# Kernel tuning notes

Hardware: AMD Instinct MI355X
Metric: run time of the kernel (lower is better)

The kernel has to match this reference:

```python
import jax, jax.numpy as jnp
import numpy as np

U = 256    # hp.hidden_size * 2 (attention num_units / encoder dim)
H = 128    # hp.hidden_size (prenet output, attn GRU input)
MEL = 80   # hp.decoder_output_dim == hp.num_mels
R = 5      # hp.outputs_per_step
B = 64
T = 1000


def _glorot(key, shape):
    fan_in = shape[-1]
    return jax.random.normal(key, shape, jnp.float32) / jnp.sqrt(jnp.float32(fan_in))


def setup_inputs() -> dict:
    key = jax.random.key(0)
    ks = jax.random.split(key, 16)
    p = {}
    p["memory"] = jax.random.normal(ks[0], (B, T, U), jnp.float32)
    # prenet: fc1 (MEL->U), fc2 (U->H)
    p["Wp1"] = _glorot(ks[1], (U, MEL)); p["bp1"] = jnp.zeros((U,), jnp.float32)
    p["Wp2"] = _glorot(ks[2], (H, U));   p["bp2"] = jnp.zeros((H,), jnp.float32)
    # Bahdanau attention params (no bias)
    p["W1"] = _glorot(ks[3], (U, U))
    p["W2"] = _glorot(ks[4], (U, U))
    p["v"]  = _glorot(ks[5], (U,))
    def gru(k, din):
        k1, k2 = jax.random.split(k)
        return (_glorot(k1, (3 * U, din)), _glorot(k2, (3 * U, U)),
                jnp.zeros((3 * U,), jnp.float32), jnp.zeros((3 * U,), jnp.float32))
    p["Wa_ih"], p["Wa_hh"], p["ba_ih"], p["ba_hh"] = gru(ks[6], H)
    p["W1_ih"], p["W1_hh"], p["b1_ih"], p["b1_hh"] = gru(ks[7], U)
    p["W2_ih"], p["W2_hh"], p["b2_ih"], p["b2_hh"] = gru(ks[8], U)
    p["Wproj"] = _glorot(ks[9], (U, 2 * U)); p["bproj"] = jnp.zeros((U,), jnp.float32)
    p["Wout"] = _glorot(ks[10], (MEL * R, U)); p["bout"] = jnp.zeros((MEL * R,), jnp.float32)
    return p


def _gru_cell(x, h, W_ih, W_hh, b_ih, b_hh):
    # torch.nn.GRUCell semantics
    gi = x @ W_ih.T + b_ih
    gh = h @ W_hh.T + b_hh
    ir, iz, inn = jnp.split(gi, 3, axis=-1)
    hr, hz, hn = jnp.split(gh, 3, axis=-1)
    r = jax.nn.sigmoid(ir + hr)
    z = jax.nn.sigmoid(iz + hz)
    n = jnp.tanh(inn + r * hn)
    return (1.0 - z) * n + z * h


def reference(memory, Wp1, bp1, Wp2, bp2, W1, W2, v,
              Wa_ih, Wa_hh, ba_ih, ba_hh,
              W1_ih, W1_hh, b1_ih, b1_hh,
              W2_ih, W2_hh, b2_ih, b2_hh,
              Wproj, bproj, Wout, bout):
    b, t, u = memory.shape
    steps = t // R  # training branch: timesteps = memory_len // outputs_per_step
    # keys = W1(memory): constant across timesteps, hoist out of the loop
    keys = jnp.einsum('btu,vu->btv', memory, W1)
    init = (jnp.zeros((b, MEL), memory.dtype),  # prev mel frame (GO frame = zeros)
            jnp.zeros((b, u), memory.dtype),    # attn_hidden
            jnp.zeros((b, u), memory.dtype),    # gru1_hidden
            jnp.zeros((b, u), memory.dtype))    # gru2_hidden

    def step(carry, _):
        prev, attn_h, g1_h, g2_h = carry
        # prenet (dropout omitted for determinism; identity in eval mode)
        x = jax.nn.relu(prev @ Wp1.T + bp1)
        x = jax.nn.relu(x @ Wp2.T + bp2)
        # attention query through GRU cell
        d_t = _gru_cell(x, attn_h, Wa_ih, Wa_hh, ba_ih, ba_hh)
        q = d_t @ W2.T                                     # [b,u]
        scores = jnp.tanh(keys + q[:, None, :]) @ v       # [b,t]
        aw = jax.nn.softmax(scores, axis=1)
        d_t_prime = jnp.einsum('bt,btu->bu', aw, memory)   # context
        # residual GRU stack
        g1_in = jnp.concatenate([d_t, d_t_prime], axis=1) @ Wproj.T + bproj
        g1_h = _gru_cell(g1_in, g1_h, W1_ih, W1_hh, b1_ih, b1_hh)
        g2_in = g1_in + g1_h
        g2_h = _gru_cell(g2_in, g2_h, W2_ih, W2_hh, b2_ih, b2_hh)
        out = ((g2_in + g2_h) @ Wout.T + bout).reshape(b, MEL, R)
        return (out[:, :, -1], d_t, g1_h, g2_h), out

    _, ys = jax.lax.scan(step, init, None, length=steps)   # [steps,b,MEL,R]
    # torch.cat(outputs, 2) -> [b, MEL, steps*R]
    return jnp.transpose(ys, (1, 2, 0, 3)).reshape(b, MEL, steps * R)
```

## Files before the change

### kernel.cpp

```cpp
#include <hip/hip_runtime.h>

typedef _Float16 f16;
typedef _Float16 h2 __attribute__((ext_vector_type(2)));
typedef float fv4 __attribute__((ext_vector_type(4)));

#define BB 64
#define UU 256
#define RRR 5
#define NQUAD 4

constexpr size_t O_WP1T = 0;
constexpr size_t O_WP2T = 10240;
constexpr size_t O_WAIH = 26624;
constexpr size_t O_WAHH = 75776;
constexpr size_t O_WQP  = 174080;
constexpr size_t O_WPC  = 239616;
constexpr size_t O_W1IH = 272384;
constexpr size_t O_W1HH = 370688;
constexpr size_t O_W2IH = 468992;
constexpr size_t O_W2HH = 567296;
constexpr size_t O_WOUT = 665600;
constexpr size_t OF_BQP = 716800;
constexpr size_t OF_W1T = 717312;
constexpr size_t OH_KEYS = 1565696;
constexpr size_t OH_MEM  = OH_KEYS + 16384000;
constexpr size_t OF_CTXP  = 17166848;
constexpr size_t OF_ESUM  = 17297920;
constexpr size_t OI_FLAGS = 17298432;

#define SCL2LOG2E 2.8853900817779268f

#if defined(__has_builtin)
#if __has_builtin(__builtin_amdgcn_fdot2)
#define USE_FDOT2 1
#endif
#endif

__device__ __forceinline__ float dot2f(h2 a, h2 b, float c){
#ifdef USE_FDOT2
  return __builtin_amdgcn_fdot2(a, b, c, false);
#else
  return c + (float)a[0]*(float)b[0] + (float)a[1]*(float)b[1];
#endif
}

__device__ __forceinline__ float frcp(float x){ return __builtin_amdgcn_rcpf(x); }
__device__ __forceinline__ float fexp2(float x){ return __builtin_amdgcn_exp2f(x); }
__device__ __forceinline__ float fsig(float x){ return frcp(1.0f + fexp2(-1.4426950408889634f*x)); }
__device__ __forceinline__ float ftanh(float x){ return 1.0f - 2.0f*frcp(1.0f + fexp2(SCL2LOG2E*x)); }

__global__ void k_tr_hx(const float* __restrict__ src, int srcK, int kbase,
                        h2* __restrict__ dst, int N, int K, int Ntot, int coloff,
                        float scale){
  int idx = blockIdx.x*blockDim.x + threadIdx.x;
  int tot = N*(K/2);
  if (idx < tot){
    int k2 = idx / N, n = idx - k2*N;
    h2 p; p[0]=(f16)(scale*src[n*srcK + kbase + 2*k2]);
    p[1]=(f16)(scale*src[n*srcK + kbase + 2*k2+1]);
    dst[(size_t)k2*Ntot + coloff + n] = p;
  }
}

__global__ void k_transpose(const float* __restrict__ src, float* __restrict__ dst, int N, int K){
  int idx = blockIdx.x*blockDim.x + threadIdx.x;
  if (idx < N*K){
    int n = idx / K, k = idx - n*K;
    dst[k*N + n] = src[idx];
  }
}

__global__ void k_biasqp(const float* __restrict__ bproj, float* __restrict__ dst){
  int i = blockIdx.x*blockDim.x + threadIdx.x;
  if (i < 512) dst[i] = (i < 256) ? 0.f : bproj[i-256];
}

__global__ void k_zero(int* __restrict__ p, int n){
  int i = blockIdx.x*blockDim.x + threadIdx.x;
  if (i < n) p[i] = 0;
}

__global__ void k_memh(const float* __restrict__ src, f16* __restrict__ dst, int n8){
  int i = blockIdx.x*blockDim.x + threadIdx.x;
  if (i < n8){
    const float4* s = reinterpret_cast<const float4*>(src) + 2*(size_t)i;
    float4 f0 = s[0], f1 = s[1];
    union { f16 h[8]; float4 v; } u;
    u.h[0]=(f16)f0.x; u.h[1]=(f16)f0.y; u.h[2]=(f16)f0.z; u.h[3]=(f16)f0.w;
    u.h[4]=(f16)f1.x; u.h[5]=(f16)f1.y; u.h[6]=(f16)f1.z; u.h[7]=(f16)f1.w;
    reinterpret_cast<float4*>(dst)[i] = u.v;
  }
}

__global__ __launch_bounds__(256) void k_keys(const float* __restrict__ mem,
      const float* __restrict__ W1t, f16* __restrict__ keys, int T)
{
  const int b = blockIdx.z;
  const int tbase = blockIdx.x * 128;
  const int cbase = blockIdx.y * 128;
  const int tid = threadIdx.x;
  const int rt = tid >> 4, ct = tid & 15;
  const float* memb = mem + (size_t)b*T*UU;

  float acc[8][8];
  #pragma unroll
  for (int i=0;i<8;i++){
    #pragma unroll
    for (int j=0;j<8;j++) acc[i][j]=0.f;
  }
  const float* arow[8];
  #pragma unroll
  for (int i=0;i<8;i++){
    int t = tbase + rt*8 + i;
    arow[i] = memb + (size_t)(t < T ? t : T-1)*UU;
  }
  const float* wcol = W1t + cbase + ct*8;

  for (int k=0;k<UU;k+=4){
    float w8[4][8];
    #pragma unroll
    for (int kk=0;kk<4;kk++){
      float4 lo = *reinterpret_cast<const float4*>(wcol + (size_t)(k+kk)*UU);
      float4 hi = *reinterpret_cast<const float4*>(wcol + (size_t)(k+kk)*UU + 4);
      w8[kk][0]=lo.x; w8[kk][1]=lo.y; w8[kk][2]=lo.z; w8[kk][3]=lo.w;
      w8[kk][4]=hi.x; w8[kk][5]=hi.y; w8[kk][6]=hi.z; w8[kk][7]=hi.w;
    }
    #pragma unroll
    for (int i=0;i<8;i++){
      float4 a = *reinterpret_cast<const float4*>(arow[i] + k);
      float a4[4] = {a.x, a.y, a.z, a.w};
      #pragma unroll
      for (int kk=0;kk<4;kk++){
        #pragma unroll
        for (int j=0;j<8;j++) acc[i][j] += a4[kk]*w8[kk][j];
      }
    }
  }
  #pragma unroll
  for (int i=0;i<8;i++){
    int t = tbase + rt*8 + i;
    if (t < T){
      f16* dst = keys + (size_t)b*T*UU + (size_t)t*UU + cbase + ct*8;
      union { f16 h[8]; float4 v; } u;
      #pragma unroll
      for (int j=0;j<8;j++) u.h[j] = (f16)(acc[i][j]*SCL2LOG2E);
      *reinterpret_cast<float4*>(dst) = u.v;
    }
  }
}

__device__ __attribute__((noinline)) void gemv_stage(
    const h2* __restrict__ W, const h2* __restrict__ in,
    const float* __restrict__ bias, float* __restrict__ dest, h2* __restrict__ desth,
    float* __restrict__ spart, int K2, int Nf4, int j4shift, int act, int tid)
{
  const int j4cap = 1 << j4shift;
  const int ksn   = 1024 >> j4shift;
  const int j4 = tid & (j4cap - 1);
  const int ks = tid >> j4shift;
  float4* part4 = reinterpret_cast<float4*>(spart);
  if (j4 < Nf4){
    int k2a = (K2 * ks) / ksn;
    int k2b = (K2 * (ks+1)) / ksn;
    const float4* w = reinterpret_cast<const float4*>(W) + (size_t)k2a * Nf4 + j4;
    float a0=0.f, a1=0.f, a2=0.f, a3=0.f;
    #pragma unroll 4
    for (int k2 = k2a; k2 < k2b; ++k2){
      float4 wp = *w; w += Nf4;
      h2 a = in[k2];
      const h2* wh = reinterpret_cast<const h2*>(&wp);
      a0 = dot2f(wh[0], a, a0);
      a1 = dot2f(wh[1], a, a1);
      a2 = dot2f(wh[2], a, a2);
      a3 = dot2f(wh[3], a, a3);
    }
    float4 r; r.x=a0; r.y=a1; r.z=a2; r.w=a3;
    part4[ks * j4cap + j4] = r;
  }
  __syncthreads();
  if (tid < Nf4){
    float4 s = part4[tid];
    for (int k = 1; k < ksn; ++k){
      float4 p = part4[k * j4cap + tid];
      s.x+=p.x; s.y+=p.y; s.z+=p.z; s.w+=p.w;
    }
    if (bias){
      float4 bv = reinterpret_cast<const float4*>(bias)[tid];
      s.x+=bv.x; s.y+=bv.y; s.z+=bv.z; s.w+=bv.w;
    }
    if (act == 1){
      s.x=fmaxf(s.x,0.f); s.y=fmaxf(s.y,0.f); s.z=fmaxf(s.z,0.f); s.w=fmaxf(s.w,0.f);
    } else if (act == 2){
      float4 d = reinterpret_cast<float4*>(dest)[tid];
      s.x+=d.x; s.y+=d.y; s.z+=d.z; s.w+=d.w;
    }
    if (dest) reinterpret_cast<float4*>(dest)[tid] = s;
    if (desth){
      h2 p0; p0[0]=(f16)s.x; p0[1]=(f16)s.y;
      h2 p1; p1[0]=(f16)s.z; p1[1]=(f16)s.w;
      desth[2*tid] = p0; desth[2*tid+1] = p1;
    }
  }
  __syncthreads();
}

__device__ __attribute__((noinline)) void gru_gate(
    const float* __restrict__ gi, const float* __restrict__ gh,
    float* __restrict__ h, h2* __restrict__ hh2,
    const float* __restrict__ addsrc, float* __restrict__ sumf,
    h2* __restrict__ sumh, int tid)
{
  if (tid < 128){
    float hn[2], sm[2] = {0.f, 0.f};
    #pragma unroll
    for (int d=0; d<2; ++d){
      int e = 2*tid + d;
      float r = fsig(gi[e] + gh[e]);
      float z = fsig(gi[256+e] + gh[256+e]);
      float n = ftanh(gi[512+e] + r*gh[512+e]);
      hn[d] = (1.f - z)*n + z*h[e];
      h[e] = hn[d];
      if (addsrc){ sm[d] = addsrc[e] + hn[d]; if (sumf) sumf[e] = sm[d]; }
    }
    h2 p; p[0]=(f16)hn[0]; p[1]=(f16)hn[1];
    hh2[tid] = p;
    if (addsrc && sumh){ h2 q; q[0]=(f16)sm[0]; q[1]=(f16)sm[1]; sumh[tid] = q; }
  }
  __syncthreads();
}

__global__ __launch_bounds__(1024) void k_decode(
    const h2* __restrict__ wts, const float* __restrict__ wsf,
    const f16* __restrict__ keysg, const f16* __restrict__ memg,
    float* __restrict__ ctxp, float* __restrict__ esum, int* __restrict__ flags,
    const float* __restrict__ bp1, const float* __restrict__ bp2,
    const float* __restrict__ vvec,
    const float* __restrict__ ba_ih, const float* __restrict__ ba_hh,
    const float* __restrict__ b1_ih, const float* __restrict__ b1_hh,
    const float* __restrict__ b2_ih, const float* __restrict__ b2_hh,
    const float* __restrict__ bout,
    float* __restrict__ out, int T, int steps)
{
  __shared__ __align__(16) float s_part[4096];
  __shared__ __align__(16) float s_sc[1024];
  __shared__ __align__(16) float s_gi[768];
  __shared__ __align__(16) float s_gh[768];
  __shared__ __align__(16) float s_gh1[768];
  __shared__ __align__(16) float s_gh2[768];
  __shared__ __align__(16) float s_q[512];
  __shared__ __align__(16) float s_ha[256];
  __shared__ __align__(16) float s_g1h[256];
  __shared__ __align__(16) float s_g2h[256];
  __shared__ __align__(16) float s_g2in[256];
  __shared__ __align__(16) float s_y[400];
  __shared__ __align__(16) f16   s_prevf[80];
  __shared__ __align__(16) h2    s_hah[128], s_g1hh[128], s_g2hh[128];
  __shared__ __align__(16) h2    s_g1inh[128], s_g2inh[128], s_s2h[128];
  __shared__ __align__(16) h2    s_x1h[128], s_xh[64], s_ctxh[128];
  __shared__ float s_wred[16];

  const int b    = blockIdx.x & 63;
  const int quad = blockIdx.x >> 6;
  const int tid = threadIdx.x;
  const int lane = tid & 63;
  const int wid = tid >> 6;
  const int half_id = lane >> 5;
  const int cl = lane & 31;

  const f16* keyb = keysg + (size_t)b*T*UU;
  const f16* memb = memg  + (size_t)b*T*UU;
  float* outb = out + (size_t)b*80*(steps*RRR);
  const int tq0 = (T*quad)/NQUAD, tq1 = (T*(quad+1))/NQUAD;

  if (tid < 128){
    s_ha[2*tid]=0.f; s_ha[2*tid+1]=0.f;
    s_g1h[2*tid]=0.f; s_g1h[2*tid+1]=0.f;
    s_g2h[2*tid]=0.f; s_g2h[2*tid+1]=0.f;
    h2 z; z[0]=(f16)0.f; z[1]=(f16)0.f;
    s_hah[tid]=z; s_g1hh[tid]=z; s_g2hh[tid]=z;
  }
  if (tid < 80) s_prevf[tid] = (f16)0.f;
  __syncthreads();

  float v8[8], m8[8];
  #pragma unroll
  for (int j=0;j<8;j++){ v8[j] = vvec[cl*8+j]; m8[j] = -2.0f*v8[j]; }
  float sumv = 0.f;
  #pragma unroll
  for (int j=0;j<8;j++) sumv += v8[j];
  #pragma unroll
  for (int o=1;o<32;o<<=1) sumv += __shfl_xor(sumv, o);

  for (int step = 0; step < steps; ++step){
    const int par = step & 1;
    gemv_stage(wts+O_WAHH, s_hah,  ba_hh, s_gh,  nullptr, s_part, 128, 192, 8, 0, tid);
    gemv_stage(wts+O_W1HH, s_g1hh, b1_hh, s_gh1, nullptr, s_part, 128, 192, 8, 0, tid);
    gemv_stage(wts+O_W2HH, s_g2hh, b2_hh, s_gh2, nullptr, s_part, 128, 192, 8, 0, tid);
    gemv_stage(wts+O_WP1T, reinterpret_cast<const h2*>(s_prevf), bp1, nullptr, s_x1h,
               s_part, 40, 64, 6, 1, tid);
    gemv_stage(wts+O_WP2T, s_x1h, bp2, nullptr, s_xh, s_part, 128, 32, 5, 1, tid);
    gemv_stage(wts+O_WAIH, s_xh, ba_ih, s_gi, nullptr, s_part, 64, 192, 8, 0, tid);
    gru_gate(s_gi, s_gh, s_ha, s_hah, nullptr, nullptr, nullptr, tid);
    gemv_stage(wts+O_WQP, s_hah, wsf+OF_BQP, s_q, nullptr, s_part, 128, 128, 7, 0, tid);

    {
      float q8[8];
      #pragma unroll
      for (int j=0;j<8;j++) q8[j] = s_q[cl*8+j];
      float rs = 0.f;
      for (int t0 = tq0 + wid*2; t0 < tq1; t0 += 32){
        int t = t0 + half_id;
        fv4 kv = *(reinterpret_cast<const fv4*>(keyb + (size_t)t*UU) + cl);
        const h2* kh = reinterpret_cast<const h2*>(&kv);
        float acc = 0.f;
        #pragma unroll
        for (int p=0;p<4;p++){
          float t0f = (float)kh[p][0] + q8[2*p];
          float t1f = (float)kh[p][1] + q8[2*p+1];
          acc = fmaf(m8[2*p],   frcp(1.f + fexp2(t0f)), acc);
          acc = fmaf(m8[2*p+1], frcp(1.f + fexp2(t1f)), acc);
        }
        #pragma unroll
        for (int o=1;o<32;o<<=1) acc += __shfl_xor(acc, o);
        float e = __expf(sumv + acc);
        if (cl == 0) s_sc[t] = e;
        rs += e;
      }
      rs += __shfl_xor(rs, 32);
      if (lane==0) s_wred[wid] = rs;
    }
    __syncthreads();
    {
      float c8[8] = {0.f,0.f,0.f,0.f,0.f,0.f,0.f,0.f};
      for (int t0 = tq0 + wid*2; t0 < tq1; t0 += 32){
        int t = t0 + half_id;
        float wgt = s_sc[t];
        fv4 mv = *(reinterpret_cast<const fv4*>(memb + (size_t)t*UU) + cl);
        const h2* mh = reinterpret_cast<const h2*>(&mv);
        #pragma unroll
        for (int p=0;p<4;p++){
          c8[2*p  ] += wgt*(float)mh[p][0];
          c8[2*p+1] += wgt*(float)mh[p][1];
        }
      }
      #pragma unroll
      for (int j=0;j<8;j++) c8[j] += __shfl_xor(c8[j], 32);
      if (half_id == 0){
        float4 lo; lo.x=c8[0]; lo.y=c8[1]; lo.z=c8[2]; lo.w=c8[3];
        float4 hi; hi.x=c8[4]; hi.y=c8[5]; hi.z=c8[6]; hi.w=c8[7];
        *reinterpret_cast<float4*>(s_part + wid*256 + cl*8)     = lo;
        *reinterpret_cast<float4*>(s_part + wid*256 + cl*8 + 4) = hi;
      }
    }
    __syncthreads();
    {
      float* cp = ctxp + (((size_t)b*2 + par)*NQUAD + quad)*256;
      if (tid < 128){
        float a = 0.f, c = 0.f;
        #pragma unroll
        for (int w=0; w<16; ++w){
          a += s_part[w*256 + 2*tid];
          c += s_part[w*256 + 2*tid+1];
        }
        cp[2*tid]   = a;
        cp[2*tid+1] = c;
      }
      if (tid == 0){
        float tot = 0.f;
        #pragma unroll
        for (int w=0; w<16; ++w) tot += s_wred[w];
        esum[((size_t)b*2 + par)*NQUAD + quad] = tot;
      }
    }
    __syncthreads();
    if (tid == 0){
      int* fl = flags + b*256 + step;
      __threadfence();
      __hip_atomic_fetch_add(fl, 1, __ATOMIC_RELEASE, __HIP_MEMORY_SCOPE_AGENT);
      while (__hip_atomic_load(fl, __ATOMIC_ACQUIRE, __HIP_MEMORY_SCOPE_AGENT) < NQUAD){
        __builtin_amdgcn_s_sleep(2);
      }
    }
    __syncthreads();
    if (tid < 128){
      const float* cp0 = ctxp + ((size_t)b*2 + par)*NQUAD*256;
      const float* es0 = esum + ((size_t)b*2 + par)*NQUAD;
      float es = 0.f;
      #pragma unroll
      for (int q4=0;q4<NQUAD;q4++)
        es += __hip_atomic_load(&es0[q4], __ATOMIC_RELAXED, __HIP_MEMORY_SCOPE_AGENT);
      float inv = frcp(es);
      float a = 0.f, c = 0.f;
      #pragma unroll
      for (int q4=0;q4<NQUAD;q4++){
        a += __hip_atomic_load(&cp0[q4*256 + 2*tid],   __ATOMIC_RELAXED, __HIP_MEMORY_SCOPE_AGENT);
        c += __hip_atomic_load(&cp0[q4*256 + 2*tid+1], __ATOMIC_RELAXED, __HIP_MEMORY_SCOPE_AGENT);
      }
      h2 p; p[0]=(f16)(a*inv); p[1]=(f16)(c*inv);
      s_ctxh[tid] = p;
    }
    __syncthreads();

    gemv_stage(wts+O_WPC, s_ctxh, nullptr, s_q+256, s_g1inh, s_part, 128, 64, 6, 2, tid);
    gemv_stage(wts+O_W1IH, s_g1inh, b1_ih, s_gi, nullptr, s_part, 128, 192, 8, 0, tid);
    gru_gate(s_gi, s_gh1, s_g1h, s_g1hh, s_q+256, s_g2in, s_g2inh, tid);
    gemv_stage(wts+O_W2IH, s_g2inh, b2_ih, s_gi, nullptr, s_part, 128, 192, 8, 0, tid);
    gru_gate(s_gi, s_gh2, s_g2h, s_g2hh, s_g2in, nullptr, s_s2h, tid);
    gemv_stage(wts+O_WOUT, s_s2h, bout, s_y, nullptr, s_part, 128, 100, 7, 0, tid);
    if (tid < 400){
      float val = s_y[tid];
      int mel = tid / 5, rr = tid - mel*5;
      if (quad == 0)
        __builtin_nontemporal_store(val, &outb[(size_t)mel*(steps*RRR) + step*RRR + rr]);
      if (rr == 4) s_prevf[mel] = (f16)val;
    }
    __syncthreads();
  }
}

extern "C" void kernel_launch(void* const* d_in, const int* in_sizes, int n_in,
                              void* d_out, int out_size, void* d_ws, size_t ws_size,
                              hipStream_t stream)
{
  const float* mem  = (const float*)d_in[0];
  const float* Wp1  = (const float*)d_in[1];
  const float* bp1  = (const float*)d_in[2];
  const float* Wp2  = (const float*)d_in[3];
  const float* bp2  = (const float*)d_in[4];
  const float* W1   = (const float*)d_in[5];
  const float* W2   = (const float*)d_in[6];
  const float* vv   = (const float*)d_in[7];
  const float* Wa_ih= (const float*)d_in[8];
  const float* Wa_hh= (const float*)d_in[9];
  const float* ba_ih= (const float*)d_in[10];
  const float* ba_hh= (const float*)d_in[11];
  const float* W1_ih= (const float*)d_in[12];
  const float* W1_hh= (const float*)d_in[13];
  const float* b1_ih= (const float*)d_in[14];
  const float* b1_hh= (const float*)d_in[15];
  const float* W2_ih= (const float*)d_in[16];
  const float* W2_hh= (const float*)d_in[17];
  const float* b2_ih= (const float*)d_in[18];
  const float* b2_hh= (const float*)d_in[19];
  const float* Wproj= (const float*)d_in[20];
  const float* bproj= (const float*)d_in[21];
  const float* Wout = (const float*)d_in[22];
  const float* bout = (const float*)d_in[23];

  h2*  wsH2 = (h2*)d_ws;
  f16* wsF16= (f16*)d_ws;
  float* wsF = (float*)d_ws;
  int*  wsI = (int*)d_ws;
  int T = in_sizes[0] / (BB*UU);
  int steps = T / RRR;

  auto tr = [&](const float* src, int srcK, int kbase, size_t off, int N, int K,
                int Ntot, int coloff, float scale){
    int total = N*(K/2);
    k_tr_hx<<<dim3((total+255)/256), dim3(256), 0, stream>>>(
        src, srcK, kbase, wsH2 + off, N, K, Ntot, coloff, scale);
  };
  tr(Wp1,   80,  0, O_WP1T, 256, 80,  256, 0, 1.f);
  tr(Wp2,   256, 0, O_WP2T, 128, 256, 128, 0, 1.f);
  tr(Wa_ih, 128, 0, O_WAIH, 768, 128, 768, 0, 1.f);
  tr(Wa_hh, 256, 0, O_WAHH, 768, 256, 768, 0, 1.f);
  tr(W2,    256, 0, O_WQP,  256, 256, 512, 0, SCL2LOG2E);
  tr(Wproj, 512, 0, O_WQP,  256, 256, 512, 256, 1.f);
  tr(Wproj, 512, 256, O_WPC, 256, 256, 256, 0, 1.f);
  tr(W1_ih, 256, 0, O_W1IH, 768, 256, 768, 0, 1.f);
  tr(W1_hh, 256, 0, O_W1HH, 768, 256, 768, 0, 1.f);
  tr(W2_ih, 256, 0, O_W2IH, 768, 256, 768, 0, 1.f);
  tr(W2_hh, 256, 0, O_W2HH, 768, 256, 768, 0, 1.f);
  tr(Wout,  256, 0, O_WOUT, 400, 256, 400, 0, 1.f);

  k_biasqp<<<dim3(2), dim3(256), 0, stream>>>(bproj, wsF + OF_BQP);
  k_transpose<<<dim3((256*256+255)/256), dim3(256), 0, stream>>>(W1, wsF + OF_W1T, 256, 256);
  k_zero<<<dim3(64), dim3(256), 0, stream>>>(wsI + OI_FLAGS, 64*256);

  int n8 = (BB*T*UU)/8;
  k_memh<<<dim3((n8+255)/256), dim3(256), 0, stream>>>(mem, wsF16 + OH_MEM, n8);
  k_keys<<<dim3((T+127)/128, UU/128, BB), dim3(256), 0, stream>>>(mem, wsF + OF_W1T, wsF16 + OH_KEYS, T);

  k_decode<<<dim3(BB*NQUAD), dim3(1024), 0, stream>>>(wsH2, wsF,
      wsF16 + OH_KEYS, wsF16 + OH_MEM,
      wsF + OF_CTXP, wsF + OF_ESUM, wsI + OI_FLAGS,
      bp1, bp2, vv, ba_ih, ba_hh, b1_ih, b1_hh, b2_ih, b2_hh, bout,
      (float*)d_out, T, steps);
}
```

Before: 12.56 ms.

## Replace LDS-reduced GEMVs with shuffle-reduced GEMVs run concurrently across thread groups

Each per-step matrix-vector product used to split K across all 1024 threads and reduce partial sums through shared memory, with two barriers per GEMV. The new version splits K only in two halves within a wavefront and combines them with a single xor-shuffle. Independent GEMVs (the hidden-state products, prenet layers) now run on disjoint thread ranges at the same time, which cuts the number of barriers per step. The cost is a much longer serial K loop per thread (64 iterations instead of a few), so each GEMV has less memory-level parallelism and more latency per thread.

```diff
diff --git a/kernel.cpp b/kernel.cpp
--- a/kernel.cpp
+++ b/kernel.cpp
@@ -149,59 +149,55 @@
   }
 }
 
-__device__ __attribute__((noinline)) void gemv_stage(
+__device__ __attribute__((noinline)) void gemv_shfl(
     const h2* __restrict__ W, const h2* __restrict__ in,
-    const float* __restrict__ bias, float* __restrict__ dest, h2* __restrict__ desth,
-    float* __restrict__ spart, int K2, int Nf4, int j4shift, int act, int tid)
+    const float* __restrict__ bias, float* __restrict__ destf, h2* __restrict__ desth,
+    int K2, int Nf4, int act, int local)
 {
-  const int j4cap = 1 << j4shift;
-  const int ksn   = 1024 >> j4shift;
-  const int j4 = tid & (j4cap - 1);
-  const int ks = tid >> j4shift;
-  float4* part4 = reinterpret_cast<float4*>(spart);
-  if (j4 < Nf4){
-    int k2a = (K2 * ks) / ksn;
-    int k2b = (K2 * (ks+1)) / ksn;
-    const float4* w = reinterpret_cast<const float4*>(W) + (size_t)k2a * Nf4 + j4;
-    float a0=0.f, a1=0.f, a2=0.f, a3=0.f;
-    #pragma unroll 4
-    for (int k2 = k2a; k2 < k2b; ++k2){
-      float4 wp = *w; w += Nf4;
-      h2 a = in[k2];
-      const h2* wh = reinterpret_cast<const h2*>(&wp);
-      a0 = dot2f(wh[0], a, a0);
-      a1 = dot2f(wh[1], a, a1);
-      a2 = dot2f(wh[2], a, a2);
-      a3 = dot2f(wh[3], a, a3);
-    }
-    float4 r; r.x=a0; r.y=a1; r.z=a2; r.w=a3;
-    part4[ks * j4cap + j4] = r;
-  }
-  __syncthreads();
-  if (tid < Nf4){
-    float4 s = part4[tid];
-    for (int k = 1; k < ksn; ++k){
-      float4 p = part4[k * j4cap + tid];
-      s.x+=p.x; s.y+=p.y; s.z+=p.z; s.w+=p.w;
-    }
+  const int lane = local & 63;
+  const int half = lane >> 5;
+  int col = (local >> 6)*32 + (lane & 31);
+  const bool valid = col < Nf4;
+  if (!valid) col = 0;
+  const int kh = K2 >> 1;
+  const float4* w = reinterpret_cast<const float4*>(W) + (size_t)(half*kh)*Nf4 + col;
+  const h2* ia = in + half*kh;
+  float a0=0.f, a1=0.f, a2=0.f, a3=0.f;
+  #pragma unroll 8
+  for (int it = 0; it < kh; ++it){
+    float4 wp = w[(size_t)it*Nf4];
+    h2 a = ia[it];
+    const h2* wh = reinterpret_cast<const h2*>(&wp);
+    a0 = dot2f(wh[0], a, a0);
+    a1 = dot2f(wh[1], a, a1);
+    a2 = dot2f(wh[2], a, a2);
+    a3 = dot2f(wh[3], a, a3);
+  }
+  a0 += __shfl_xor(a0, 32, 64);
+  a1 += __shfl_xor(a1, 32, 64);
+  a2 += __shfl_xor(a2, 32, 64);
+  a3 += __shfl_xor(a3, 32, 64);
+  if (half == 0 && valid){
     if (bias){
-      float4 bv = reinterpret_cast<const float4*>(bias)[tid];
-      s.x+=bv.x; s.y+=bv.y; s.z+=bv.z; s.w+=bv.w;
+      const float4 bv = reinterpret_cast<const float4*>(bias)[col];
+      a0+=bv.x; a1+=bv.y; a2+=bv.z; a3+=bv.w;
     }
     if (act == 1){
-      s.x=fmaxf(s.x,0.f); s.y=fmaxf(s.y,0.f); s.z=fmaxf(s.z,0.f); s.w=fmaxf(s.w,0.f);
+      a0=fmaxf(a0,0.f); a1=fmaxf(a1,0.f); a2=fmaxf(a2,0.f); a3=fmaxf(a3,0.f);
     } else if (act == 2){
-      float4 d = reinterpret_cast<float4*>(dest)[tid];
-      s.x+=d.x; s.y+=d.y; s.z+=d.z; s.w+=d.w;
-    }
-    if (dest) reinterpret_cast<float4*>(dest)[tid] = s;
+      const float4 d = reinterpret_cast<float4*>(destf)[col];
+      a0+=d.x; a1+=d.y; a2+=d.z; a3+=d.w;
+    }
+    if (destf){
+      float4 r; r.x=a0; r.y=a1; r.z=a2; r.w=a3;
+      reinterpret_cast<float4*>(destf)[col] = r;
+    }
     if (desth){
-      h2 p0; p0[0]=(f16)s.x; p0[1]=(f16)s.y;
-      h2 p1; p1[0]=(f16)s.z; p1[1]=(f16)s.w;
-      desth[2*tid] = p0; desth[2*tid+1] = p1;
-    }
-  }
-  __syncthreads();
+      h2 p0; p0[0]=(f16)a0; p0[1]=(f16)a1;
+      h2 p1; p1[0]=(f16)a2; p1[1]=(f16)a3;
+      desth[2*col] = p0; desth[2*col+1] = p1;
+    }
+  }
 }
 
 __device__ __attribute__((noinline)) void gru_gate(
@@ -241,7 +237,7 @@
     const float* __restrict__ bout,
     float* __restrict__ out, int T, int steps)
 {
-  __shared__ __align__(16) float s_part[4096];
+  __shared__ __align__(16) float s_red[4096];
   __shared__ __align__(16) float s_sc[1024];
   __shared__ __align__(16) float s_gi[768];
   __shared__ __align__(16) float s_gh[768];
@@ -293,15 +289,19 @@
 
   for (int step = 0; step < steps; ++step){
     const int par = step & 1;
-    gemv_stage(wts+O_WAHH, s_hah,  ba_hh, s_gh,  nullptr, s_part, 128, 192, 8, 0, tid);
-    gemv_stage(wts+O_W1HH, s_g1hh, b1_hh, s_gh1, nullptr, s_part, 128, 192, 8, 0, tid);
-    gemv_stage(wts+O_W2HH, s_g2hh, b2_hh, s_gh2, nullptr, s_part, 128, 192, 8, 0, tid);
-    gemv_stage(wts+O_WP1T, reinterpret_cast<const h2*>(s_prevf), bp1, nullptr, s_x1h,
-               s_part, 40, 64, 6, 1, tid);
-    gemv_stage(wts+O_WP2T, s_x1h, bp2, nullptr, s_xh, s_part, 128, 32, 5, 1, tid);
-    gemv_stage(wts+O_WAIH, s_xh, ba_ih, s_gi, nullptr, s_part, 64, 192, 8, 0, tid);
+    if (tid < 384)      gemv_shfl(wts+O_WAHH, s_hah,  ba_hh, s_gh,  nullptr, 128, 192, 0, tid);
+    else if (tid < 768) gemv_shfl(wts+O_W1HH, s_g1hh, b1_hh, s_gh1, nullptr, 128, 192, 0, tid-384);
+    else if (tid < 896) gemv_shfl(wts+O_WP1T, reinterpret_cast<const h2*>(s_prevf), bp1,
+                                  nullptr, s_x1h, 40, 64, 1, tid-768);
+    __syncthreads();
+    if (tid < 384)      gemv_shfl(wts+O_W2HH, s_g2hh, b2_hh, s_gh2, nullptr, 128, 192, 0, tid);
+    else if (tid < 448) gemv_shfl(wts+O_WP2T, s_x1h, bp2, nullptr, s_xh, 128, 32, 1, tid-384);
+    __syncthreads();
+    if (tid < 384) gemv_shfl(wts+O_WAIH, s_xh, ba_ih, s_gi, nullptr, 64, 192, 0, tid);
+    __syncthreads();
     gru_gate(s_gi, s_gh, s_ha, s_hah, nullptr, nullptr, nullptr, tid);
-    gemv_stage(wts+O_WQP, s_hah, wsf+OF_BQP, s_q, nullptr, s_part, 128, 128, 7, 0, tid);
+    if (tid < 256) gemv_shfl(wts+O_WQP, s_hah, wsf+OF_BQP, s_q, nullptr, 128, 128, 0, tid);
+    __syncthreads();
 
     {
       float q8[8];
@@ -348,8 +348,8 @@
       if (half_id == 0){
         float4 lo; lo.x=c8[0]; lo.y=c8[1]; lo.z=c8[2]; lo.w=c8[3];
         float4 hi; hi.x=c8[4]; hi.y=c8[5]; hi.z=c8[6]; hi.w=c8[7];
-        *reinterpret_cast<float4*>(s_part + wid*256 + cl*8)     = lo;
-        *reinterpret_cast<float4*>(s_part + wid*256 + cl*8 + 4) = hi;
+        *reinterpret_cast<float4*>(s_red + wid*256 + cl*8)     = lo;
+        *reinterpret_cast<float4*>(s_red + wid*256 + cl*8 + 4) = hi;
       }
     }
     __syncthreads();
@@ -359,8 +359,8 @@
         float a = 0.f, c = 0.f;
         #pragma unroll
         for (int w=0; w<16; ++w){
-          a += s_part[w*256 + 2*tid];
-          c += s_part[w*256 + 2*tid+1];
+          a += s_red[w*256 + 2*tid];
+          c += s_red[w*256 + 2*tid+1];
         }
         cp[2*tid]   = a;
         cp[2*tid+1] = c;
@@ -401,12 +401,16 @@
     }
     __syncthreads();
 
-    gemv_stage(wts+O_WPC, s_ctxh, nullptr, s_q+256, s_g1inh, s_part, 128, 64, 6, 2, tid);
-    gemv_stage(wts+O_W1IH, s_g1inh, b1_ih, s_gi, nullptr, s_part, 128, 192, 8, 0, tid);
+    if (tid < 128) gemv_shfl(wts+O_WPC, s_ctxh, nullptr, s_q+256, s_g1inh, 128, 64, 2, tid);
+    __syncthreads();
+    if (tid < 384) gemv_shfl(wts+O_W1IH, s_g1inh, b1_ih, s_gi, nullptr, 128, 192, 0, tid);
+    __syncthreads();
     gru_gate(s_gi, s_gh1, s_g1h, s_g1hh, s_q+256, s_g2in, s_g2inh, tid);
-    gemv_stage(wts+O_W2IH, s_g2inh, b2_ih, s_gi, nullptr, s_part, 128, 192, 8, 0, tid);
+    if (tid < 384) gemv_shfl(wts+O_W2IH, s_g2inh, b2_ih, s_gi, nullptr, 128, 192, 0, tid);
+    __syncthreads();
     gru_gate(s_gi, s_gh2, s_g2h, s_g2hh, s_g2in, nullptr, s_s2h, tid);
-    gemv_stage(wts+O_WOUT, s_s2h, bout, s_y, nullptr, s_part, 128, 100, 7, 0, tid);
+    if (tid < 256) gemv_shfl(wts+O_WOUT, s_s2h, bout, s_y, nullptr, 128, 100, 0, tid);
+    __syncthreads();
     if (tid < 400){
       float val = s_y[tid];
       int mel = tid / 5, rr = tid - mel*5;
```

New measurement: 12.43 ms. Within noise of the previous version (-1.0%).
